# Performance work log

Hardware: AMD Instinct MI355X
Metric: run time of the kernel (lower is better)

## Reference

```python
import jax, jax.numpy as jnp
import numpy as np

D = 256
EXP = 4


def layer_norm(x, gamma, beta, eps=1e-5):
    mu = jnp.mean(x, axis=-1, keepdims=True)
    var = jnp.var(x, axis=-1, keepdims=True)
    return (x - mu) / jnp.sqrt(var + eps) * gamma + beta


def setup_inputs() -> dict:
    key = jax.random.key(0)
    ks = jax.random.split(key, 7)
    B, N = 8, 2048
    x = jax.random.normal(ks[0], (B, N, D), dtype=jnp.float32)
    w1 = jax.random.normal(ks[1], (D, EXP * D), dtype=jnp.float32) * (1.0 / np.sqrt(D))
    b1 = jnp.zeros((EXP * D,), dtype=jnp.float32)
    w2 = jax.random.normal(ks[2], (EXP * D, D), dtype=jnp.float32) * (1.0 / np.sqrt(EXP * D))
    b2 = jnp.zeros((D,), dtype=jnp.float32)
    g1 = jnp.ones((D,), dtype=jnp.float32)
    be1 = jnp.zeros((D,), dtype=jnp.float32)
    g2 = jnp.ones((D,), dtype=jnp.float32)
    be2 = jnp.zeros((D,), dtype=jnp.float32)
    return {"x": x, "w1": w1, "b1": b1, "w2": w2, "b2": b2,
            "gamma1": g1, "beta1": be1, "gamma2": g2, "beta2": be2}


def reference(x, w1, b1, w2, b2, gamma1, beta1, gamma2, beta2):
    # Sublayer 1: x + SA(LN(x)); SA uses raw QK^T softmax with Q=K=V=LN(x)
    h = layer_norm(x, gamma1, beta1)               # [B,N,D]
    scale = jnp.sqrt(jnp.float32(h.shape[-1]))
    scores = jnp.einsum('bnd,bmd->bnm', h, h) / scale  # [B,N,N]
    prob = jax.nn.softmax(scores, axis=-1)
    sa_out = jnp.einsum('bnm,bmd->bnd', prob, h)
    x = x + sa_out
    # Sublayer 2: x + FFN(LN(x))
    h2 = layer_norm(x, gamma2, beta2)
    ffn = jax.nn.relu(h2 @ w1 + b1) @ w2 + b2
    return x + ffn
```

## Files before the change

### kernel.cpp

```cpp
#include <hip/hip_runtime.h>
#include <hip/hip_bf16.h>

typedef unsigned short u16;
typedef __attribute__((ext_vector_type(8))) short short8;
typedef __attribute__((ext_vector_type(4))) float f32x4;

typedef unsigned int __attribute__((address_space(1))) as1_u32;
typedef unsigned int __attribute__((address_space(3))) as3_u32;

__device__ __forceinline__ void gload16(const void* g, void* l) {
    __builtin_amdgcn_global_load_lds((const as1_u32*)g, (as3_u32*)l, 16, 0, 0);
}

__device__ __forceinline__ u16 f2b(float f) {
    union { float f; unsigned u; } v; v.f = f;
    unsigned r = v.u + 0x7fffu + ((v.u >> 16) & 1u);
    return (u16)(r >> 16);
}

__global__ void transpose_cast(const float* __restrict__ src,
                               u16* __restrict__ dst, int R, int C) {
    __shared__ float tile[32][33];
    const int c0 = blockIdx.x * 32, r0 = blockIdx.y * 32;
    const int tx = threadIdx.x, ty = threadIdx.y;
#pragma unroll
    for (int i = ty; i < 32; i += 8)
        tile[i][tx] = src[(size_t)(r0 + i) * C + c0 + tx];
    __syncthreads();
#pragma unroll
    for (int i = ty; i < 32; i += 8)
        dst[(size_t)(c0 + i) * R + r0 + tx] = f2b(tile[tx][i]);
}

__global__ void transpose_bf16(const u16* __restrict__ src, u16* __restrict__ dst) {
    __shared__ u16 t[32][33];
    const int b = blockIdx.z;
    const int n0 = blockIdx.x * 32, d0 = blockIdx.y * 32;
    const int tx = threadIdx.x, ty = threadIdx.y;
    const u16* s = src + (size_t)b * (2048 * 256);
    u16* d = dst + (size_t)b * (2048 * 256);
#pragma unroll
    for (int i = ty; i < 32; i += 8)
        t[i][tx] = s[(size_t)(n0 + i) * 256 + d0 + tx];
    __syncthreads();
#pragma unroll
    for (int i = ty; i < 32; i += 8)
        d[(size_t)(d0 + i) * 2048 + n0 + tx] = t[tx][i];
}

__global__ __launch_bounds__(256) void ln_kernel(
    const float* __restrict__ x, const float* __restrict__ g,
    const float* __restrict__ be, u16* __restrict__ out) {
    const int lane = threadIdx.x & 63;
    const size_t row = (size_t)blockIdx.x * 4 + (threadIdx.x >> 6);
    const float4 v = *((const float4*)(x + row * 256) + lane);
    float s  = v.x + v.y + v.z + v.w;
    float s2 = v.x * v.x + v.y * v.y + v.z * v.z + v.w * v.w;
#pragma unroll
    for (int m = 1; m < 64; m <<= 1) {
        s  += __shfl_xor(s, m);
        s2 += __shfl_xor(s2, m);
    }
    const float mean = s * (1.0f / 256.0f);
    const float var  = s2 * (1.0f / 256.0f) - mean * mean;
    const float rstd = rsqrtf(var + 1e-5f);
    const float4 gv = *((const float4*)g + lane);
    const float4 bv = *((const float4*)be + lane);
    ushort4 o;
    o.x = f2b((v.x - mean) * rstd * gv.x + bv.x);
    o.y = f2b((v.y - mean) * rstd * gv.y + bv.y);
    o.z = f2b((v.z - mean) * rstd * gv.z + bv.z);
    o.w = f2b((v.w - mean) * rstd * gv.w + bv.w);
    *((ushort4*)(out + row * 256) + lane) = o;
}

#define ATTN_LDS_BYTES (2*65536 + 8*16*40*2)

__global__ __launch_bounds__(512) void attn_kernel(
    const u16* __restrict__ h, const u16* __restrict__ hT,
    const float* __restrict__ x, float* __restrict__ xmid) {
    extern __shared__ char smem[];
    const int tid  = threadIdx.x;
    const int w    = tid >> 6;
    const int lane = tid & 63;
    const int grp  = lane >> 4;
    const int l16  = lane & 15;
    const int qsub = w & 3;
    const int kh   = w >> 2;
    const int b    = blockIdx.y;
    const int q0   = blockIdx.x * 64;

    const u16* hb = h + (size_t)b * (2048 * 256);
    const char* hbB = (const char*)hb;
    const char* hTB = (const char*)(hT + (size_t)b * (2048 * 256));
    u16* myP = (u16*)(smem + 131072) + w * (16 * 40);

    short8 qf[8];
    {
        const u16* qp = hb + (size_t)(q0 + qsub * 16 + l16) * 256 + grp * 8;
#pragma unroll
        for (int kk = 0; kk < 8; ++kk) qf[kk] = *(const short8*)(qp + kk * 32);
    }

    f32x4 oacc[16];
#pragma unroll
    for (int n = 0; n < 16; ++n) oacc[n] = (f32x4){0.f, 0.f, 0.f, 0.f};
    float m_run[4] = {-1e30f, -1e30f, -1e30f, -1e30f};
    float l_run[4] = {0.f, 0.f, 0.f, 0.f};

    const char* gK0 = hbB + ((size_t)(tid >> 5) << 9)
                          + (((tid & 31) ^ ((tid >> 5) & 7)) << 4);
    const char* gV0 = hTB + ((size_t)(tid >> 3) << 12)
                          + (((tid & 7) ^ ((tid >> 3) & 7)) << 4);

    {
        char* lK = smem + w * 1024;
        char* lV = smem + 32768 + w * 1024;
#pragma unroll
        for (int it = 0; it < 4; ++it) gload16(gK0 + (size_t)it * 8192, lK + it * 8192);
#pragma unroll
        for (int it = 0; it < 4; ++it) gload16(gV0 + (size_t)it * 262144, lV + it * 8192);
    }
    __syncthreads();

    for (int kt = 0; kt < 32; ++kt) {
        const int cur = kt & 1;
        if (kt < 31) {
            char* lK = smem + (cur ^ 1) * 65536 + w * 1024;
            char* lV = smem + (cur ^ 1) * 65536 + 32768 + w * 1024;
            const char* gK = gK0 + (size_t)(kt + 1) * 32768;
            const char* gV = gV0 + (size_t)(kt + 1) * 128;
#pragma unroll
            for (int it = 0; it < 4; ++it) gload16(gK + (size_t)it * 8192, lK + it * 8192);
#pragma unroll
            for (int it = 0; it < 4; ++it) gload16(gV + (size_t)it * 262144, lV + it * 8192);
        }
        const char* KBb = smem + cur * 65536;
        const char* VBb = KBb + 32768;

        f32x4 sacc[2];
#pragma unroll
        for (int j = 0; j < 2; ++j) sacc[j] = (f32x4){0.f, 0.f, 0.f, 0.f};
#pragma unroll
        for (int j = 0; j < 2; ++j) {
            const char* rb = KBb + ((kh * 32 + j * 16 + l16) << 9);
#pragma unroll
            for (int kk = 0; kk < 8; ++kk) {
                const int c = grp + 4 * kk;
                const int swz = (c & ~7) | ((c ^ l16) & 7);
                sacc[j] = __builtin_amdgcn_mfma_f32_16x16x32_bf16(
                    qf[kk], *(const short8*)(rb + (swz << 4)), sacc[j], 0, 0, 0);
            }
        }

        float sv[2][4];
#pragma unroll
        for (int j = 0; j < 2; ++j)
#pragma unroll
            for (int r = 0; r < 4; ++r) sv[j][r] = sacc[j][r] * 0.0625f;
        float tmax[4];
#pragma unroll
        for (int r = 0; r < 4; ++r) {
            float m = fmaxf(sv[0][r], sv[1][r]);
            m = fmaxf(m, __shfl_xor(m, 1));
            m = fmaxf(m, __shfl_xor(m, 2));
            m = fmaxf(m, __shfl_xor(m, 4));
            m = fmaxf(m, __shfl_xor(m, 8));
            tmax[r] = m;
        }
        const bool need = (tmax[0] > m_run[0] + 8.f) || (tmax[1] > m_run[1] + 8.f) ||
                          (tmax[2] > m_run[2] + 8.f) || (tmax[3] > m_run[3] + 8.f);
        if (__any(need)) {
#pragma unroll
            for (int r = 0; r < 4; ++r) {
                const float mnew  = fmaxf(m_run[r], tmax[r]);
                const float alpha = __expf(m_run[r] - mnew);
                m_run[r] = mnew;
                l_run[r] *= alpha;
#pragma unroll
                for (int n = 0; n < 16; ++n) oacc[n][r] *= alpha;
            }
        }
#pragma unroll
        for (int r = 0; r < 4; ++r) {
            float lt = 0.f;
#pragma unroll
            for (int j = 0; j < 2; ++j) {
                const float p = __expf(sv[j][r] - m_run[r]);
                lt += p;
                myP[(grp * 4 + r) * 40 + j * 16 + l16] = f2b(p);
            }
            lt += __shfl_xor(lt, 1);
            lt += __shfl_xor(lt, 2);
            lt += __shfl_xor(lt, 4);
            lt += __shfl_xor(lt, 8);
            l_run[r] += lt;
        }

        {
            const short8 pa = *(const short8*)(myP + l16 * 40 + grp * 8);
            const int cc2 = ((kh << 2) + grp) ^ (l16 & 7);
#pragma unroll
            for (int n = 0; n < 16; ++n) {
                const short8 bv =
                    *(const short8*)(VBb + ((n * 16 + l16) << 7) + (cc2 << 4));
                oacc[n] = __builtin_amdgcn_mfma_f32_16x16x32_bf16(pa, bv, oacc[n], 0, 0, 0);
            }
        }
        __syncthreads();
    }

    const int pair = w & 3;
    if (w >= 4) {
#pragma unroll
        for (int n = 0; n < 16; ++n)
            *(f32x4*)(smem + pair * 16384 + (n * 16 + l16) * 64 + grp * 16) = oacc[n];
        if (l16 == 0) {
            float* mlp = (float*)(smem + 131072 + pair * 128);
#pragma unroll
            for (int r = 0; r < 4; ++r) {
                mlp[(grp * 4 + r) * 2]     = m_run[r];
                mlp[(grp * 4 + r) * 2 + 1] = l_run[r];
            }
        }
    }
    __syncthreads();
    if (w < 4) {
        float c0[4], c1[4];
        {
            const float* mlp = (const float*)(smem + 131072 + w * 128);
#pragma unroll
            for (int r = 0; r < 4; ++r) {
                const float m1 = mlp[(grp * 4 + r) * 2];
                const float l1 = mlp[(grp * 4 + r) * 2 + 1];
                const float M  = fmaxf(m_run[r], m1);
                const float a0 = __expf(m_run[r] - M);
                const float a1 = __expf(m1 - M);
                const float inv = 1.0f / (l_run[r] * a0 + l1 * a1);
                c0[r] = a0 * inv;
                c1[r] = a1 * inv;
            }
        }
        const float* xb = x + (size_t)b * (2048 * 256);
        float* ob = xmid + (size_t)b * (2048 * 256);
#pragma unroll
        for (int n = 0; n < 16; ++n) {
            const f32x4 o1 = *(const f32x4*)(smem + w * 16384 + (n * 16 + l16) * 64 + grp * 16);
#pragma unroll
            for (int r = 0; r < 4; ++r) {
                const int row = q0 + w * 16 + grp * 4 + r;
                const size_t idx = (size_t)row * 256 + n * 16 + l16;
                ob[idx] = xb[idx] + oacc[n][r] * c0[r] + o1[r] * c1[r];
            }
        }
    }
}

#define FFN_LDS_BYTES (2*65536 + 8*16*40*2)

__global__ __launch_bounds__(512) void ffn_kernel(
    const u16* __restrict__ h2, const u16* __restrict__ w1t,
    const u16* __restrict__ w2t, const float* __restrict__ b1,
    const float* __restrict__ b2, float* __restrict__ xmid) {
    extern __shared__ char smem[];
    const int tid  = threadIdx.x;
    const int w    = tid >> 6;
    const int lane = tid & 63;
    const int grp  = lane >> 4;
    const int l16  = lane & 15;
    const int qsub = w & 3;
    const int hh   = w >> 2;
    const int t0   = blockIdx.x * 64;
    u16* myA = (u16*)(smem + 131072) + w * (16 * 40);

    short8 af[8];
    {
        const u16* ap = h2 + (size_t)(t0 + qsub * 16 + l16) * 256 + grp * 8;
#pragma unroll
        for (int kk = 0; kk < 8; ++kk) af[kk] = *(const short8*)(ap + kk * 32);
    }

    f32x4 oacc[16];
#pragma unroll
    for (int n = 0; n < 16; ++n) oacc[n] = (f32x4){0.f, 0.f, 0.f, 0.f};

    const char* g10 = (const char*)w1t + ((size_t)(tid >> 5) << 9)
                                       + (((tid & 31) ^ ((tid >> 5) & 7)) << 4);
    const char* g20 = (const char*)w2t + ((size_t)(tid >> 3) << 11)
                                       + (((tid & 7) ^ ((tid >> 3) & 7)) << 4);

    {
        char* l1 = smem + w * 1024;
        char* l2 = smem + 32768 + w * 1024;
#pragma unroll
        for (int it = 0; it < 4; ++it) gload16(g10 + (size_t)it * 8192, l1 + it * 8192);
#pragma unroll
        for (int it = 0; it < 4; ++it) gload16(g20 + (size_t)it * 131072, l2 + it * 8192);
    }
    __syncthreads();

    for (int hc = 0; hc < 16; ++hc) {
        const int cur = hc & 1;
        if (hc < 15) {
            char* l1 = smem + (cur ^ 1) * 65536 + w * 1024;
            char* l2 = smem + (cur ^ 1) * 65536 + 32768 + w * 1024;
            const char* g1 = g10 + (size_t)(hc + 1) * 32768;
            const char* g2 = g20 + (size_t)(hc + 1) * 128;
#pragma unroll
            for (int it = 0; it < 4; ++it) gload16(g1 + (size_t)it * 8192, l1 + it * 8192);
#pragma unroll
            for (int it = 0; it < 4; ++it) gload16(g2 + (size_t)it * 131072, l2 + it * 8192);
        }
        const char* W1b = smem + cur * 65536;
        const char* W2b = W1b + 32768;

        f32x4 sacc[2];
#pragma unroll
        for (int j = 0; j < 2; ++j) sacc[j] = (f32x4){0.f, 0.f, 0.f, 0.f};
#pragma unroll
        for (int j = 0; j < 2; ++j) {
            const char* rb = W1b + ((hh * 32 + j * 16 + l16) << 9);
#pragma unroll
            for (int kk = 0; kk < 8; ++kk) {
                const int c = grp + 4 * kk;
                const int swz = (c & ~7) | ((c ^ l16) & 7);
                sacc[j] = __builtin_amdgcn_mfma_f32_16x16x32_bf16(
                    af[kk], *(const short8*)(rb + (swz << 4)), sacc[j], 0, 0, 0);
            }
        }

#pragma unroll
        for (int j = 0; j < 2; ++j) {
            const float bias = b1[hc * 64 + hh * 32 + j * 16 + l16];
#pragma unroll
            for (int r = 0; r < 4; ++r) {
                const float v = fmaxf(sacc[j][r] + bias, 0.f);
                myA[(grp * 4 + r) * 40 + j * 16 + l16] = f2b(v);
            }
        }

        {
            const short8 pa = *(const short8*)(myA + l16 * 40 + grp * 8);
            const int cc2 = ((hh << 2) + grp) ^ (l16 & 7);
#pragma unroll
            for (int n = 0; n < 16; ++n) {
                const short8 bv =
                    *(const short8*)(W2b + ((n * 16 + l16) << 7) + (cc2 << 4));
                oacc[n] = __builtin_amdgcn_mfma_f32_16x16x32_bf16(pa, bv, oacc[n], 0, 0, 0);
            }
        }
        __syncthreads();
    }

    const int pair = w & 3;
    if (w >= 4) {
#pragma unroll
        for (int n = 0; n < 16; ++n)
            *(f32x4*)(smem + pair * 16384 + (n * 16 + l16) * 64 + grp * 16) = oacc[n];
    }
    __syncthreads();
    if (w < 4) {
#pragma unroll
        for (int n = 0; n < 16; ++n) {
            const f32x4 o1 = *(const f32x4*)(smem + w * 16384 + (n * 16 + l16) * 64 + grp * 16);
            const float bias2 = b2[n * 16 + l16];
#pragma unroll
            for (int r = 0; r < 4; ++r) {
                const int row = t0 + w * 16 + grp * 4 + r;
                const size_t idx = (size_t)row * 256 + n * 16 + l16;
                xmid[idx] = xmid[idx] + oacc[n][r] + o1[r] + bias2;
            }
        }
    }
}

extern "C" void kernel_launch(void* const* d_in, const int* in_sizes, int n_in,
                              void* d_out, int out_size, void* d_ws, size_t ws_size,
                              hipStream_t stream) {
    (void)in_sizes; (void)n_in; (void)out_size; (void)ws_size;
    const float* x   = (const float*)d_in[0];
    const float* w1  = (const float*)d_in[1];
    const float* b1  = (const float*)d_in[2];
    const float* w2  = (const float*)d_in[3];
    const float* b2  = (const float*)d_in[4];
    const float* g1  = (const float*)d_in[5];
    const float* be1 = (const float*)d_in[6];
    const float* g2  = (const float*)d_in[7];
    const float* be2 = (const float*)d_in[8];
    float* out = (float*)d_out;

    char* ws = (char*)d_ws;
    u16* h   = (u16*)ws;
    u16* hT  = (u16*)(ws + 8388608);
    u16* w1t = (u16*)(ws + 16777216);
    u16* w2t = (u16*)(ws + 17301504);

    hipFuncSetAttribute((const void*)attn_kernel,
                        hipFuncAttributeMaxDynamicSharedMemorySize, ATTN_LDS_BYTES);
    hipFuncSetAttribute((const void*)ffn_kernel,
                        hipFuncAttributeMaxDynamicSharedMemorySize, FFN_LDS_BYTES);

    transpose_cast<<<dim3(32, 8), dim3(32, 8), 0, stream>>>(w1, w1t, 256, 1024);
    transpose_cast<<<dim3(8, 32), dim3(32, 8), 0, stream>>>(w2, w2t, 1024, 256);

    ln_kernel<<<4096, 256, 0, stream>>>(x, g1, be1, h);
    transpose_bf16<<<dim3(64, 8, 8), dim3(32, 8), 0, stream>>>(h, hT);
    attn_kernel<<<dim3(32, 8), 512, ATTN_LDS_BYTES, stream>>>(h, hT, x, out);

    ln_kernel<<<4096, 256, 0, stream>>>(out, g2, be2, h);
    ffn_kernel<<<256, 512, FFN_LDS_BYTES, stream>>>(h, w1t, w2t, b1, b2, out);
}
```

Before: 216.9 us.

## Swap MFMA operands so each lane holds one query row in softmax

```diff
diff --git a/kernel.cpp b/kernel.cpp
--- a/kernel.cpp
+++ b/kernel.cpp
@@ -2,6 +2,7 @@
 #include <hip/hip_bf16.h>
 
 typedef unsigned short u16;
+typedef unsigned int u32;
 typedef __attribute__((ext_vector_type(8))) short short8;
 typedef __attribute__((ext_vector_type(4))) float f32x4;
 
@@ -93,7 +94,7 @@
     const u16* hb = h + (size_t)b * (2048 * 256);
     const char* hbB = (const char*)hb;
     const char* hTB = (const char*)(hT + (size_t)b * (2048 * 256));
-    u16* myP = (u16*)(smem + 131072) + w * (16 * 40);
+    char* myPb = smem + 131072 + w * 1280;
 
     short8 qf[8];
     {
@@ -105,8 +106,8 @@
     f32x4 oacc[16];
 #pragma unroll
     for (int n = 0; n < 16; ++n) oacc[n] = (f32x4){0.f, 0.f, 0.f, 0.f};
-    float m_run[4] = {-1e30f, -1e30f, -1e30f, -1e30f};
-    float l_run[4] = {0.f, 0.f, 0.f, 0.f};
+    float m_run = -1e30f;
+    float l_run = 0.f;
 
     const char* gK0 = hbB + ((size_t)(tid >> 5) << 9)
                           + (((tid & 31) ^ ((tid >> 5) & 7)) << 4);
@@ -149,56 +150,57 @@
                 const int c = grp + 4 * kk;
                 const int swz = (c & ~7) | ((c ^ l16) & 7);
                 sacc[j] = __builtin_amdgcn_mfma_f32_16x16x32_bf16(
-                    qf[kk], *(const short8*)(rb + (swz << 4)), sacc[j], 0, 0, 0);
-            }
-        }
-
-        float sv[2][4];
+                    *(const short8*)(rb + (swz << 4)), qf[kk], sacc[j], 0, 0, 0);
+            }
+        }
+
+        float p[2][4];
 #pragma unroll
         for (int j = 0; j < 2; ++j)
 #pragma unroll
-            for (int r = 0; r < 4; ++r) sv[j][r] = sacc[j][r] * 0.0625f;
-        float tmax[4];
-#pragma unroll
-        for (int r = 0; r < 4; ++r) {
-            float m = fmaxf(sv[0][r], sv[1][r]);
-            m = fmaxf(m, __shfl_xor(m, 1));
-            m = fmaxf(m, __shfl_xor(m, 2));
-            m = fmaxf(m, __shfl_xor(m, 4));
-            m = fmaxf(m, __shfl_xor(m, 8));
-            tmax[r] = m;
-        }
-        const bool need = (tmax[0] > m_run[0] + 8.f) || (tmax[1] > m_run[1] + 8.f) ||
-                          (tmax[2] > m_run[2] + 8.f) || (tmax[3] > m_run[3] + 8.f);
-        if (__any(need)) {
+            for (int r = 0; r < 4; ++r) p[j][r] = sacc[j][r] * 0.0625f;
+        float m = p[0][0];
+#pragma unroll
+        for (int j = 0; j < 2; ++j)
+#pragma unroll
+            for (int r = 0; r < 4; ++r) m = fmaxf(m, p[j][r]);
+        m = fmaxf(m, __shfl_xor(m, 16));
+        m = fmaxf(m, __shfl_xor(m, 32));
+        if (__any(m > m_run + 8.f)) {
+            const float mnew  = fmaxf(m_run, m);
+            const float alpha = __expf(m_run - mnew);
+            m_run = mnew;
+            l_run *= alpha;
+            float ar[4];
+#pragma unroll
+            for (int r = 0; r < 4; ++r) ar[r] = __shfl(alpha, grp * 4 + r);
+#pragma unroll
+            for (int n = 0; n < 16; ++n)
+#pragma unroll
+                for (int r = 0; r < 4; ++r) oacc[n][r] *= ar[r];
+        }
+        float lt = 0.f;
+#pragma unroll
+        for (int j = 0; j < 2; ++j)
 #pragma unroll
             for (int r = 0; r < 4; ++r) {
-                const float mnew  = fmaxf(m_run[r], tmax[r]);
-                const float alpha = __expf(m_run[r] - mnew);
-                m_run[r] = mnew;
-                l_run[r] *= alpha;
-#pragma unroll
-                for (int n = 0; n < 16; ++n) oacc[n][r] *= alpha;
-            }
-        }
-#pragma unroll
-        for (int r = 0; r < 4; ++r) {
-            float lt = 0.f;
-#pragma unroll
-            for (int j = 0; j < 2; ++j) {
-                const float p = __expf(sv[j][r] - m_run[r]);
-                lt += p;
-                myP[(grp * 4 + r) * 40 + j * 16 + l16] = f2b(p);
-            }
-            lt += __shfl_xor(lt, 1);
-            lt += __shfl_xor(lt, 2);
-            lt += __shfl_xor(lt, 4);
-            lt += __shfl_xor(lt, 8);
-            l_run[r] += lt;
-        }
+                p[j][r] = __expf(p[j][r] - m_run);
+                lt += p[j][r];
+            }
+        lt += __shfl_xor(lt, 16);
+        lt += __shfl_xor(lt, 32);
+        l_run += lt;
+
+#pragma unroll
+        for (int j = 0; j < 2; ++j)
+#pragma unroll
+            for (int rp = 0; rp < 2; ++rp) {
+                const u32 pk = (u32)f2b(p[j][rp * 2]) | ((u32)f2b(p[j][rp * 2 + 1]) << 16);
+                *(u32*)(myPb + l16 * 80 + (j * 16 + grp * 4 + rp * 2) * 2) = pk;
+            }
 
         {
-            const short8 pa = *(const short8*)(myP + l16 * 40 + grp * 8);
+            const short8 pa = *(const short8*)(myPb + l16 * 80 + grp * 16);
             const int cc2 = ((kh << 2) + grp) ^ (l16 & 7);
 #pragma unroll
             for (int n = 0; n < 16; ++n) {
@@ -215,13 +217,10 @@
 #pragma unroll
         for (int n = 0; n < 16; ++n)
             *(f32x4*)(smem + pair * 16384 + (n * 16 + l16) * 64 + grp * 16) = oacc[n];
-        if (l16 == 0) {
+        if (lane < 16) {
             float* mlp = (float*)(smem + 131072 + pair * 128);
-#pragma unroll
-            for (int r = 0; r < 4; ++r) {
-                mlp[(grp * 4 + r) * 2]     = m_run[r];
-                mlp[(grp * 4 + r) * 2 + 1] = l_run[r];
-            }
+            mlp[l16 * 2]     = m_run;
+            mlp[l16 * 2 + 1] = l_run;
         }
     }
     __syncthreads();
@@ -231,12 +230,14 @@
             const float* mlp = (const float*)(smem + 131072 + w * 128);
 #pragma unroll
             for (int r = 0; r < 4; ++r) {
+                const float m0 = __shfl(m_run, grp * 4 + r);
+                const float l0 = __shfl(l_run, grp * 4 + r);
                 const float m1 = mlp[(grp * 4 + r) * 2];
                 const float l1 = mlp[(grp * 4 + r) * 2 + 1];
-                const float M  = fmaxf(m_run[r], m1);
-                const float a0 = __expf(m_run[r] - M);
+                const float M  = fmaxf(m0, m1);
+                const float a0 = __expf(m0 - M);
                 const float a1 = __expf(m1 - M);
-                const float inv = 1.0f / (l_run[r] * a0 + l1 * a1);
+                const float inv = 1.0f / (l0 * a0 + l1 * a1);
                 c0[r] = a0 * inv;
                 c1[r] = a1 * inv;
             }
@@ -256,7 +257,7 @@
     }
 }
 
-#define FFN_LDS_BYTES (2*65536 + 8*16*40*2)
+#define FFN_LDS_BYTES (2*65536 + 8*16*40*2 + 4096)
 
 __global__ __launch_bounds__(512) void ffn_kernel(
     const u16* __restrict__ h2, const u16* __restrict__ w1t,
@@ -271,7 +272,8 @@
     const int qsub = w & 3;
     const int hh   = w >> 2;
     const int t0   = blockIdx.x * 64;
-    u16* myA = (u16*)(smem + 131072) + w * (16 * 40);
+    char* myAb = smem + 131072 + w * 1280;
+    const char* b1lds = smem + 141312;
 
     short8 af[8];
     {
@@ -296,6 +298,8 @@
         for (int it = 0; it < 4; ++it) gload16(g10 + (size_t)it * 8192, l1 + it * 8192);
 #pragma unroll
         for (int it = 0; it < 4; ++it) gload16(g20 + (size_t)it * 131072, l2 + it * 8192);
+        if (tid < 256)
+            gload16((const char*)b1 + tid * 16, (char*)b1lds + tid * 16);
     }
     __syncthreads();
 
@@ -325,22 +329,24 @@
                 const int c = grp + 4 * kk;
                 const int swz = (c & ~7) | ((c ^ l16) & 7);
                 sacc[j] = __builtin_amdgcn_mfma_f32_16x16x32_bf16(
-                    af[kk], *(const short8*)(rb + (swz << 4)), sacc[j], 0, 0, 0);
+                    *(const short8*)(rb + (swz << 4)), af[kk], sacc[j], 0, 0, 0);
             }
         }
 
 #pragma unroll
         for (int j = 0; j < 2; ++j) {
-            const float bias = b1[hc * 64 + hh * 32 + j * 16 + l16];
-#pragma unroll
-            for (int r = 0; r < 4; ++r) {
-                const float v = fmaxf(sacc[j][r] + bias, 0.f);
-                myA[(grp * 4 + r) * 40 + j * 16 + l16] = f2b(v);
+            const f32x4 bj = *(const f32x4*)(b1lds + (hc * 64 + hh * 32 + j * 16 + grp * 4) * 4);
+#pragma unroll
+            for (int rp = 0; rp < 2; ++rp) {
+                const float v0 = fmaxf(sacc[j][rp * 2]     + bj[rp * 2],     0.f);
+                const float v1 = fmaxf(sacc[j][rp * 2 + 1] + bj[rp * 2 + 1], 0.f);
+                const u32 pk = (u32)f2b(v0) | ((u32)f2b(v1) << 16);
+                *(u32*)(myAb + l16 * 80 + (j * 16 + grp * 4 + rp * 2) * 2) = pk;
             }
         }
 
         {
-            const short8 pa = *(const short8*)(myA + l16 * 40 + grp * 8);
+            const short8 pa = *(const short8*)(myAb + l16 * 80 + grp * 16);
             const int cc2 = ((hh << 2) + grp) ^ (l16 & 7);
 #pragma unroll
             for (int n = 0; n < 16; ++n) {
```

Result: faster. 198.0 us (-8.7%).
